# Performance work log

Measured on AMD Instinct MI355X. Metric: run time of the kernel, lower is better.

Reference implementation:

```python
import jax, jax.numpy as jnp
import numpy as np

H1, H2 = 80, 100

def _lstm_layer(x, W_ih, W_hh, b_ih, b_hh):
    # x: [B,T,D]; W_ih: [4H,D]; W_hh: [4H,H]; gate order i,f,g,o (PyTorch)
    B, T, _ = x.shape
    H = W_hh.shape[1]
    xg = jnp.einsum('btd,gd->btg', x, W_ih) + b_ih + b_hh  # [B,T,4H]
    def step(carry, xg_t):
        h, c = carry
        g = xg_t + h @ W_hh.T
        i = jax.nn.sigmoid(g[:, 0*H:1*H])
        f = jax.nn.sigmoid(g[:, 1*H:2*H])
        gg = jnp.tanh(g[:, 2*H:3*H])
        o = jax.nn.sigmoid(g[:, 3*H:4*H])
        c = f * c + i * gg
        h = o * jnp.tanh(c)
        return (h, c), h
    h0 = jnp.zeros((B, H), x.dtype)
    (_, _), hs = jax.lax.scan(step, (h0, h0), jnp.swapaxes(xg, 0, 1))
    return jnp.swapaxes(hs, 0, 1)  # [B,T,H]

def setup_inputs() -> dict:
    key = jax.random.key(0)
    ks = jax.random.split(key, 13)
    def u(k, shape, fan):
        s = 1.0 / np.sqrt(fan)
        return jax.random.uniform(k, shape, jnp.float32, -s, s)
    B, T = 1024, 512
    return {
        'x': jax.random.normal(ks[0], (B, T, 1), jnp.float32),
        'W_ih1': u(ks[1], (4*H1, 1), H1), 'W_hh1': u(ks[2], (4*H1, H1), H1),
        'b_ih1': u(ks[3], (4*H1,), H1), 'b_hh1': u(ks[4], (4*H1,), H1),
        'W_ih2': u(ks[5], (4*H2, H1), H2), 'W_hh2': u(ks[6], (4*H2, H2), H2),
        'b_ih2': u(ks[7], (4*H2,), H2), 'b_hh2': u(ks[8], (4*H2,), H2),
        'W_l1': u(ks[9], (10, 100), 100), 'b_l1': u(ks[10], (10,), 100),
        'W_l2': u(ks[11], (1, 10), 10), 'b_l2': u(ks[12], (1,), 10),
    }

def reference(x, W_ih1, W_hh1, b_ih1, b_hh1, W_ih2, W_hh2, b_ih2, b_hh2, W_l1, b_l1, W_l2, b_l2):
    h = jax.nn.relu(_lstm_layer(x, W_ih1, W_hh1, b_ih1, b_hh1))
    h = jax.nn.relu(_lstm_layer(h, W_ih2, W_hh2, b_ih2, b_hh2))
    h = h[:, -1, :]                       # [B,100]
    h = jax.nn.relu(h @ W_l1.T + b_l1)    # [B,10]
    return h @ W_l2.T + b_l2              # [B,1]
```

## Files before the change

kernel.cpp:

```cpp
#include <hip/hip_runtime.h>
#include <hip/hip_bf16.h>

#define T_STEPS 512
#define BATCH   1024
#define HD1     80
#define HD2     100
#define NB2     16

#define NKT1    3
#define NUT1    5
#define NT1     (4 * NUT1)
#define NKT2    6
#define NUT2    7
#define NT2     (4 * NUT2)
#define W1F_DW  (NT1 * NKT1 * 64 * 4)
#define W2F_DW  (NT2 * NKT2 * 64 * 4)

typedef _Float16 half2_t __attribute__((ext_vector_type(2)));
typedef _Float16 f16x4   __attribute__((ext_vector_type(4)));
typedef _Float16 f16x8   __attribute__((ext_vector_type(8)));
typedef float    f32x4   __attribute__((ext_vector_type(4)));

union HU { unsigned int u; half2_t h; };
static __device__ __forceinline__ unsigned int packh(float a, float b) {
    HU x; x.h.x = (_Float16)a; x.h.y = (_Float16)b; return x.u;
}

static __device__ __forceinline__ float sigm(float z) {
    return __builtin_amdgcn_rcpf(1.f + __expf(-z));
}
static __device__ __forceinline__ float tanhf_(float z) {
    return fmaf(2.f, __builtin_amdgcn_rcpf(1.f + __expf(-2.f * z)), -1.f);
}

__global__ __launch_bounds__(256)
void prep_kernel(const float* __restrict__ W_hh1,
                 const float* __restrict__ W_ih2,
                 const float* __restrict__ W_hh2,
                 const float* __restrict__ W_ih1,
                 const float* __restrict__ b_ih1,
                 const float* __restrict__ b_hh1,
                 const float* __restrict__ b_ih2,
                 const float* __restrict__ b_hh2,
                 unsigned int* __restrict__ w1f,
                 unsigned int* __restrict__ w2f)
{
    int i = blockIdx.x * 256 + threadIdx.x;
    if (i < W1F_DW) {
        int H  = 2 * i;
        int s  = H & 7;
        int l  = (H >> 3) & 63;
        int ri = H >> 9;
        int kt = ri % NKT1;
        int tile = ri / NKT1;
        int g  = tile / NUT1, j = tile % NUT1;
        int r  = g * HD1 + j * 16 + (l & 15);
        int k  = kt * 32 + (l >> 4) * 8 + s;
        auto val1 = [&](int kk) -> float {
            if (kk < HD1) return W_hh1[r * HD1 + kk];
            if (kk == HD1) return b_ih1[r] + b_hh1[r];
            if (kk == HD1 + 1) return W_ih1[r];
            return 0.f;
        };
        w1f[i] = packh(val1(k), val1(k + 1));
    } else if (i < W1F_DW + W2F_DW) {
        int d  = i - W1F_DW;
        int H  = 2 * d;
        int s  = H & 7;
        int l  = (H >> 3) & 63;
        int ri = H >> 9;
        int kt = ri % NKT2;
        int tile = ri / NKT2;
        int g  = tile / NUT2, j = tile % NUT2;
        int up = j * 16 + (l & 15);
        int k  = kt * 32 + (l >> 4) * 8 + s;
        float v0 = 0.f, v1 = 0.f;
        if (up < HD2) {
            int r = g * HD2 + up;
            auto val2 = [&](int kk) -> float {
                if (kk < HD1) return W_ih2[r * HD1 + kk];
                if (kk < HD1 + HD2) return W_hh2[r * HD2 + (kk - HD1)];
                if (kk == HD1 + HD2) return b_ih2[r] + b_hh2[r];
                return 0.f;
            };
            v0 = val2(k); v1 = val2(k + 1);
        }
        w2f[d] = packh(v0, v1);
    }
}

__global__ __launch_bounds__(768, 1)
void lstm_fused(const float* __restrict__ x,
                const _Float16* __restrict__ w1f,
                const _Float16* __restrict__ w2f,
                float* __restrict__ h2last)
{
    const int tid = threadIdx.x;
    const int l   = tid & 63;
    const int wv  = tid >> 6;
    const int b0  = blockIdx.x * NB2;
    const int bt  = l & 15;
    const int ro  = (l >> 4) << 2;
    const bool isL2 = (wv < 7);
    const int lane_base = ((l >> 4) << 7) + (bt << 3);

    __shared__ float    xs[T_STEPS * NB2];
    __shared__ _Float16 h1b[2][12 * 128];
    __shared__ _Float16 Hb[2][24 * 128];

    f16x8 a[4][NKT2];
    if (isL2) {
#pragma unroll
        for (int g = 0; g < 4; g++)
#pragma unroll
            for (int kt = 0; kt < NKT2; kt++)
                a[g][kt] = *(const volatile f16x8*)(w2f +
                    ((size_t)((g * NUT2 + wv) * NKT2 + kt) * 64 + l) * 8);
    } else {
        const int j1 = wv - 7;
#pragma unroll
        for (int g = 0; g < 4; g++)
#pragma unroll
            for (int kt = 0; kt < NKT1; kt++)
                a[g][kt] = *(const volatile f16x8*)(w1f +
                    ((size_t)((g * NUT1 + j1) * NKT1 + kt) * 64 + l) * 8);
    }

    const int u0 = isL2 ? (wv * 16 + ro) : ((wv - 7) * 16 + ro);
    const bool worker = isL2 ? (u0 < HD2) : true;

    float c[4] = {0.f, 0.f, 0.f, 0.f};

    for (int i = tid; i < 2 * 12 * 128 / 2; i += 768) ((unsigned int*)h1b)[i] = 0u;
    for (int i = tid; i < 2 * 24 * 128 / 2; i += 768) ((unsigned int*)Hb)[i]  = 0u;
    for (int idx = tid; idx < T_STEPS * NB2; idx += 768) {
        int tt = idx & (T_STEPS - 1), bb = idx >> 9;
        xs[tt * NB2 + bb] = x[((size_t)(b0 + bb)) * T_STEPS + tt];
    }
    __syncthreads();
    if (tid < NB2) {
        h1b[0][10 * 128 + tid * 8 + 0] = (_Float16)1.f;
        h1b[1][10 * 128 + tid * 8 + 0] = (_Float16)1.f;
        h1b[1][10 * 128 + tid * 8 + 1] =
            (_Float16)x[((size_t)(b0 + tid)) * T_STEPS];
        Hb[0][22 * 128 + tid * 8 + 4] = (_Float16)1.f;
        Hb[1][22 * 128 + tid * 8 + 4] = (_Float16)1.f;
    }
    __syncthreads();

#pragma unroll 2
    for (int i = 0; i <= T_STEPS; i++) {
        const int rp = (i - 1) & 1;
        const int wp = i & 1;
        if (isL2) {
            if (i >= 1) {
                const _Float16* bp = &Hb[rp][0] + lane_base;
                f16x8 bfr[NKT2];
#pragma unroll
                for (int kt = 0; kt < NKT2; kt++)
                    bfr[kt] = *(const f16x8*)(bp + kt * 512);
                f32x4 acc[4];
#pragma unroll
                for (int g = 0; g < 4; g++) {
                    f32x4 z4 = {0.f, 0.f, 0.f, 0.f};
#pragma unroll
                    for (int kt = 0; kt < NKT2; kt++)
                        z4 = __builtin_amdgcn_mfma_f32_16x16x32_f16(
                                 a[g][kt], bfr[kt], z4, 0, 0, 0);
                    acc[g] = z4;
                }
                if (worker) {
                    f16x4 hh;
#pragma unroll
                    for (int r = 0; r < 4; r++) {
                        float gi = sigm(acc[0][r]);
                        float gf = sigm(acc[1][r]);
                        float gg = tanhf_(acc[2][r]);
                        float go = sigm(acc[3][r]);
                        c[r] = fmaf(gf, c[r], gi * gg);
                        float h = go * tanhf_(c[r]);
                        hh[r] = (_Float16)h;
                        if (i == T_STEPS)
                            h2last[(size_t)(b0 + bt) * HD2 + u0 + r] = fmaxf(h, 0.f);
                    }
                    int k0 = HD1 + u0;
                    *(f16x4*)&Hb[wp][(k0 >> 3) * 128 + (bt << 3) + (k0 & 7)] = hh;
                }
            }
        } else {
            if (i < T_STEPS) {
                const _Float16* bp = &h1b[rp][0] + lane_base;
                f16x8 bfr[NKT1];
#pragma unroll
                for (int kt = 0; kt < NKT1; kt++)
                    bfr[kt] = *(const f16x8*)(bp + kt * 512);
                f32x4 acc[4];
#pragma unroll
                for (int g = 0; g < 4; g++) {
                    f32x4 z4 = {0.f, 0.f, 0.f, 0.f};
#pragma unroll
                    for (int kt = 0; kt < NKT1; kt++)
                        z4 = __builtin_amdgcn_mfma_f32_16x16x32_f16(
                                 a[g][kt], bfr[kt], z4, 0, 0, 0);
                    acc[g] = z4;
                }
                f16x4 hraw, hrel;
#pragma unroll
                for (int r = 0; r < 4; r++) {
                    float gi = sigm(acc[0][r]);
                    float gf = sigm(acc[1][r]);
                    float gg = tanhf_(acc[2][r]);
                    float go = sigm(acc[3][r]);
                    c[r] = fmaf(gf, c[r], gi * gg);
                    float h = go * tanhf_(c[r]);
                    hraw[r] = (_Float16)h;
                    hrel[r] = (_Float16)fmaxf(h, 0.f);
                }
                int off = (u0 >> 3) * 128 + (bt << 3) + (u0 & 7);
                *(f16x4*)&h1b[wp][off] = hraw;
                *(f16x4*)&Hb[wp][off]  = hrel;
                if (wv == 7 && l < NB2 && i + 1 < T_STEPS)
                    h1b[wp][10 * 128 + l * 8 + 1] =
                        (_Float16)xs[(i + 1) * NB2 + l];
            }
        }
        __syncthreads();
    }
}

__global__ __launch_bounds__(64)
void head_kernel(const float* __restrict__ h2last,
                 const float* __restrict__ W_l1,
                 const float* __restrict__ b_l1,
                 const float* __restrict__ W_l2,
                 const float* __restrict__ b_l2,
                 float* __restrict__ out)
{
    int b = blockIdx.x * 64 + threadIdx.x;
    if (b >= BATCH) return;
    const float* h = h2last + (size_t)b * HD2;
    float o = b_l2[0];
#pragma unroll
    for (int u = 0; u < 10; u++) {
        float s = b_l1[u];
#pragma unroll
        for (int k = 0; k < HD2; k++) s = fmaf(W_l1[u * HD2 + k], h[k], s);
        o = fmaf(W_l2[u], fmaxf(s, 0.f), o);
    }
    out[b] = o;
}

extern "C" void kernel_launch(void* const* d_in, const int* in_sizes, int n_in,
                              void* d_out, int out_size, void* d_ws, size_t ws_size,
                              hipStream_t stream)
{
    const float* x     = (const float*)d_in[0];
    const float* W_ih1 = (const float*)d_in[1];
    const float* W_hh1 = (const float*)d_in[2];
    const float* b_ih1 = (const float*)d_in[3];
    const float* b_hh1 = (const float*)d_in[4];
    const float* W_ih2 = (const float*)d_in[5];
    const float* W_hh2 = (const float*)d_in[6];
    const float* b_ih2 = (const float*)d_in[7];
    const float* b_hh2 = (const float*)d_in[8];
    const float* W_l1  = (const float*)d_in[9];
    const float* b_l1  = (const float*)d_in[10];
    const float* W_l2  = (const float*)d_in[11];
    const float* b_l2  = (const float*)d_in[12];
    float* out = (float*)d_out;

    char* p = (char*)d_ws;
    float* h2last      = (float*)p;        p += (size_t)BATCH * HD2 * 4;
    unsigned int* w1fu = (unsigned int*)p; p += (size_t)W1F_DW * 4;
    unsigned int* w2fu = (unsigned int*)p;

    int prep_n = W1F_DW + W2F_DW;
    hipLaunchKernelGGL(prep_kernel, dim3((prep_n + 255) / 256), dim3(256), 0, stream,
                       W_hh1, W_ih2, W_hh2, W_ih1, b_ih1, b_hh1, b_ih2, b_hh2,
                       w1fu, w2fu);
    hipLaunchKernelGGL(lstm_fused, dim3(BATCH / NB2), dim3(768), 0, stream,
                       x, (const _Float16*)w1fu, (const _Float16*)w2fu, h2last);
    hipLaunchKernelGGL(head_kernel, dim3(BATCH / 64), dim3(64), 0, stream,
                       h2last, W_l1, b_l1, W_l2, b_l2, out);
}
```

Measured before the change: 681.2 us.

## Split LSTM layers into producer/consumer blocks pipelined through global memory with flags

Replaces the single fused block per batch group, which ran both LSTM layers in lockstep with 12 waves, with separate layer-1 and layer-2 blocks. The layer-1 block writes ReLU'd hidden states to global memory in 16-step chunks and publishes a per-chunk ready flag. The layer-2 block has a loader wave that polls these flags and prefetches chunks into double-buffered LDS using global_load_lds. The aim is to let each layer run on its own CU with less per-step barrier contention, doubling the number of blocks to use more of the GPU. The cost is extra global traffic, spin-wait latency, and a dependence on producer and consumer blocks being co-resident to avoid deadlock.

```diff
diff --git a/kernel.cpp b/kernel.cpp
--- a/kernel.cpp
+++ b/kernel.cpp
@@ -6,6 +6,7 @@
 #define HD1     80
 #define HD2     100
 #define NB2     16
+#define NGRP    (BATCH / NB2)
 
 #define NKT1    3
 #define NUT1    5
@@ -16,6 +17,10 @@
 #define W1F_DW  (NT1 * NKT1 * 64 * 4)
 #define W2F_DW  (NT2 * NKT2 * 64 * 4)
 
+#define CH      16
+#define NCH     (T_STEPS / CH)
+#define LINE_H  1280
+
 typedef _Float16 half2_t __attribute__((ext_vector_type(2)));
 typedef _Float16 f16x4   __attribute__((ext_vector_type(4)));
 typedef _Float16 f16x8   __attribute__((ext_vector_type(8)));
@@ -31,6 +36,12 @@
 }
 static __device__ __forceinline__ float tanhf_(float z) {
     return fmaf(2.f, __builtin_amdgcn_rcpf(1.f + __expf(-2.f * z)), -1.f);
+}
+
+static __device__ __forceinline__ void gld_lds16(const void* g, void* l) {
+    __builtin_amdgcn_global_load_lds(
+        (const __attribute__((address_space(1))) unsigned int*)g,
+        (__attribute__((address_space(3))) unsigned int*)l, 16, 0, 0);
 }
 
 __global__ __launch_bounds__(256)
@@ -43,7 +54,8 @@
                  const float* __restrict__ b_ih2,
                  const float* __restrict__ b_hh2,
                  unsigned int* __restrict__ w1f,
-                 unsigned int* __restrict__ w2f)
+                 unsigned int* __restrict__ w2f,
+                 int* __restrict__ flags)
 {
     int i = blockIdx.x * 256 + threadIdx.x;
     if (i < W1F_DW) {
@@ -86,88 +98,167 @@
             v0 = val2(k); v1 = val2(k + 1);
         }
         w2f[d] = packh(v0, v1);
+    } else if (i < W1F_DW + W2F_DW + NGRP * NCH) {
+        flags[i - W1F_DW - W2F_DW] = 0;
     }
 }
 
-__global__ __launch_bounds__(768, 1)
-void lstm_fused(const float* __restrict__ x,
+__global__ __launch_bounds__(512, 1)
+void lstm_split(const float* __restrict__ x,
                 const _Float16* __restrict__ w1f,
                 const _Float16* __restrict__ w2f,
+                _Float16* __restrict__ h1g,
+                int* __restrict__ flags,
                 float* __restrict__ h2last)
 {
     const int tid = threadIdx.x;
     const int l   = tid & 63;
     const int wv  = tid >> 6;
-    const int b0  = blockIdx.x * NB2;
     const int bt  = l & 15;
     const int ro  = (l >> 4) << 2;
-    const bool isL2 = (wv < 7);
     const int lane_base = ((l >> 4) << 7) + (bt << 3);
 
     __shared__ float    xs[T_STEPS * NB2];
     __shared__ _Float16 h1b[2][12 * 128];
-    __shared__ _Float16 Hb[2][24 * 128];
-
-    f16x8 a[4][NKT2];
-    if (isL2) {
-#pragma unroll
-        for (int g = 0; g < 4; g++)
-#pragma unroll
-            for (int kt = 0; kt < NKT2; kt++)
-                a[g][kt] = *(const volatile f16x8*)(w2f +
-                    ((size_t)((g * NUT2 + wv) * NKT2 + kt) * 64 + l) * 8);
-    } else {
-        const int j1 = wv - 7;
-#pragma unroll
-        for (int g = 0; g < 4; g++)
-#pragma unroll
-            for (int kt = 0; kt < NKT1; kt++)
-                a[g][kt] = *(const volatile f16x8*)(w1f +
-                    ((size_t)((g * NUT1 + j1) * NKT1 + kt) * 64 + l) * 8);
-    }
-
-    const int u0 = isL2 ? (wv * 16 + ro) : ((wv - 7) * 16 + ro);
-    const bool worker = isL2 ? (u0 < HD2) : true;
-
-    float c[4] = {0.f, 0.f, 0.f, 0.f};
-
-    for (int i = tid; i < 2 * 12 * 128 / 2; i += 768) ((unsigned int*)h1b)[i] = 0u;
-    for (int i = tid; i < 2 * 24 * 128 / 2; i += 768) ((unsigned int*)Hb)[i]  = 0u;
-    for (int idx = tid; idx < T_STEPS * NB2; idx += 768) {
-        int tt = idx & (T_STEPS - 1), bb = idx >> 9;
-        xs[tt * NB2 + bb] = x[((size_t)(b0 + bb)) * T_STEPS + tt];
-    }
-    __syncthreads();
-    if (tid < NB2) {
-        h1b[0][10 * 128 + tid * 8 + 0] = (_Float16)1.f;
-        h1b[1][10 * 128 + tid * 8 + 0] = (_Float16)1.f;
-        h1b[1][10 * 128 + tid * 8 + 1] =
-            (_Float16)x[((size_t)(b0 + tid)) * T_STEPS];
-        Hb[0][22 * 128 + tid * 8 + 4] = (_Float16)1.f;
-        Hb[1][22 * 128 + tid * 8 + 4] = (_Float16)1.f;
-    }
-    __syncthreads();
+    __shared__ _Float16 chunkbuf[2][CH * LINE_H];
+    __shared__ _Float16 h2buf[2][14 * 128];
+
+    if (blockIdx.x < NGRP) {
+        const int g  = blockIdx.x;
+        const int b0 = g * NB2;
+        const bool workerW = (wv < 5);
+        const int u0 = wv * 16 + ro;
+
+        f16x8 a[4][NKT1];
+        if (workerW) {
+#pragma unroll
+            for (int gg = 0; gg < 4; gg++)
+#pragma unroll
+                for (int kt = 0; kt < NKT1; kt++)
+                    a[gg][kt] = *(const volatile f16x8*)(w1f +
+                        ((size_t)((gg * NUT1 + wv) * NKT1 + kt) * 64 + l) * 8);
+        }
+        float c[4] = {0.f, 0.f, 0.f, 0.f};
+
+        for (int i = tid; i < 2 * 12 * 128 / 2; i += 512) ((unsigned int*)h1b)[i] = 0u;
+        for (int idx = tid; idx < T_STEPS * NB2; idx += 512) {
+            int tt = idx & (T_STEPS - 1), bb = idx >> 9;
+            xs[tt * NB2 + bb] = x[((size_t)(b0 + bb)) * T_STEPS + tt];
+        }
+        __syncthreads();
+        if (tid < NB2) {
+            h1b[0][10 * 128 + tid * 8 + 0] = (_Float16)1.f;
+            h1b[1][10 * 128 + tid * 8 + 0] = (_Float16)1.f;
+            h1b[1][10 * 128 + tid * 8 + 1] = (_Float16)xs[0 * NB2 + tid];
+        }
+        __syncthreads();
 
 #pragma unroll 2
-    for (int i = 0; i <= T_STEPS; i++) {
-        const int rp = (i - 1) & 1;
-        const int wp = i & 1;
-        if (isL2) {
-            if (i >= 1) {
-                const _Float16* bp = &Hb[rp][0] + lane_base;
-                f16x8 bfr[NKT2];
-#pragma unroll
-                for (int kt = 0; kt < NKT2; kt++)
+        for (int i = 0; i < T_STEPS; i++) {
+            const int rp = (i - 1) & 1, wp = i & 1;
+            if (workerW) {
+                const _Float16* bp = &h1b[rp][0] + lane_base;
+                f16x8 bfr[NKT1];
+#pragma unroll
+                for (int kt = 0; kt < NKT1; kt++)
                     bfr[kt] = *(const f16x8*)(bp + kt * 512);
                 f32x4 acc[4];
 #pragma unroll
-                for (int g = 0; g < 4; g++) {
+                for (int gg = 0; gg < 4; gg++) {
+                    f32x4 z4 = {0.f, 0.f, 0.f, 0.f};
+#pragma unroll
+                    for (int kt = 0; kt < NKT1; kt++)
+                        z4 = __builtin_amdgcn_mfma_f32_16x16x32_f16(
+                                 a[gg][kt], bfr[kt], z4, 0, 0, 0);
+                    acc[gg] = z4;
+                }
+                f16x4 hraw, hrel;
+#pragma unroll
+                for (int r = 0; r < 4; r++) {
+                    float gi = sigm(acc[0][r]);
+                    float gf = sigm(acc[1][r]);
+                    float gg2 = tanhf_(acc[2][r]);
+                    float go = sigm(acc[3][r]);
+                    c[r] = fmaf(gf, c[r], gi * gg2);
+                    float h = go * tanhf_(c[r]);
+                    hraw[r] = (_Float16)h;
+                    hrel[r] = (_Float16)fmaxf(h, 0.f);
+                }
+                int off = (u0 >> 3) * 128 + (bt << 3) + (u0 & 7);
+                *(f16x4*)&h1b[wp][off] = hraw;
+                size_t goff = (((size_t)(i >> 4) * NGRP + g) * CH + (i & 15)) * LINE_H + off;
+                *(f16x4*)(h1g + goff) = hrel;
+            } else if (wv == 5 && l < NB2 && i + 1 < T_STEPS) {
+                h1b[wp][10 * 128 + l * 8 + 1] = (_Float16)xs[(i + 1) * NB2 + l];
+            }
+            __syncthreads();
+            if ((i & 15) == 15 && tid == 0) {
+                __threadfence();
+                __hip_atomic_store(&flags[g * NCH + (i >> 4)], 1,
+                                   __ATOMIC_RELEASE, __HIP_MEMORY_SCOPE_AGENT);
+            }
+        }
+    } else {
+        const int g  = blockIdx.x - NGRP;
+        const int b0 = g * NB2;
+        const bool workerWave = (wv < 7);
+        const int u0 = wv * 16 + ro;
+        const bool worker = workerWave && (u0 < HD2);
+
+        f16x8 a[4][NKT2];
+        if (workerWave) {
+#pragma unroll
+            for (int gg = 0; gg < 4; gg++)
+#pragma unroll
+                for (int kt = 0; kt < NKT2; kt++)
+                    a[gg][kt] = *(const volatile f16x8*)(w2f +
+                        ((size_t)((gg * NUT2 + wv) * NKT2 + kt) * 64 + l) * 8);
+        }
+        float c[4] = {0.f, 0.f, 0.f, 0.f};
+
+        for (int i = tid; i < 2 * 14 * 128 / 2; i += 512) ((unsigned int*)h2buf)[i] = 0u;
+        __syncthreads();
+        if (tid < NB2) {
+            h2buf[0][12 * 128 + tid * 8 + 4] = (_Float16)1.f;
+            h2buf[1][12 * 128 + tid * 8 + 4] = (_Float16)1.f;
+        }
+        if (wv == 7) {
+            while (__hip_atomic_load(&flags[g * NCH], __ATOMIC_ACQUIRE,
+                                     __HIP_MEMORY_SCOPE_AGENT) == 0)
+                __builtin_amdgcn_s_sleep(8);
+            const _Float16* gsrc = h1g + (size_t)g * (CH * LINE_H) + l * 8;
+#pragma unroll
+            for (int q = 0; q < 40; q++)
+                gld_lds16(gsrc + q * 512, &chunkbuf[0][q * 512]);
+        }
+        __syncthreads();
+
+        int cb = 0;
+        bool nissued = false;
+        for (int i = 0; i < T_STEPS; i++) {
+            const int tc = i & (CH - 1);
+            const int ch = i >> 4;
+            if (workerWave) {
+                const _Float16* ck  = &chunkbuf[cb][tc * LINE_H];
+                const _Float16* h2p = &h2buf[i & 1][0];
+                f16x8 bfr[NKT2];
+#pragma unroll
+                for (int kt = 0; kt < NKT2; kt++) {
+                    int gi = kt * 4 + (l >> 4);
+                    const _Float16* src = (gi < 10)
+                        ? (ck + gi * 128 + (bt << 3))
+                        : (h2p + (gi - 10) * 128 + (bt << 3));
+                    bfr[kt] = *(const f16x8*)src;
+                }
+                f32x4 acc[4];
+#pragma unroll
+                for (int gg = 0; gg < 4; gg++) {
                     f32x4 z4 = {0.f, 0.f, 0.f, 0.f};
 #pragma unroll
                     for (int kt = 0; kt < NKT2; kt++)
                         z4 = __builtin_amdgcn_mfma_f32_16x16x32_f16(
-                                 a[g][kt], bfr[kt], z4, 0, 0, 0);
-                    acc[g] = z4;
+                                 a[gg][kt], bfr[kt], z4, 0, 0, 0);
+                    acc[gg] = z4;
                 }
                 if (worker) {
                     f16x4 hh;
@@ -175,56 +266,42 @@
                     for (int r = 0; r < 4; r++) {
                         float gi = sigm(acc[0][r]);
                         float gf = sigm(acc[1][r]);
-                        float gg = tanhf_(acc[2][r]);
+                        float gg2 = tanhf_(acc[2][r]);
                         float go = sigm(acc[3][r]);
-                        c[r] = fmaf(gf, c[r], gi * gg);
+                        c[r] = fmaf(gf, c[r], gi * gg2);
                         float h = go * tanhf_(c[r]);
                         hh[r] = (_Float16)h;
-                        if (i == T_STEPS)
+                        if (i == T_STEPS - 1)
                             h2last[(size_t)(b0 + bt) * HD2 + u0 + r] = fmaxf(h, 0.f);
                     }
                     int k0 = HD1 + u0;
-                    *(f16x4*)&Hb[wp][(k0 >> 3) * 128 + (bt << 3) + (k0 & 7)] = hh;
+                    *(f16x4*)&h2buf[(i + 1) & 1]
+                        [((k0 >> 3) - 10) * 128 + (bt << 3) + (k0 & 7)] = hh;
+                }
+            } else {
+                if (!nissued && ch + 1 < NCH) {
+                    bool rdy = (__hip_atomic_load(&flags[g * NCH + ch + 1],
+                                    __ATOMIC_ACQUIRE, __HIP_MEMORY_SCOPE_AGENT) != 0);
+                    if (tc == CH - 1 && !rdy) {
+                        while (__hip_atomic_load(&flags[g * NCH + ch + 1],
+                                   __ATOMIC_ACQUIRE, __HIP_MEMORY_SCOPE_AGENT) == 0)
+                            __builtin_amdgcn_s_sleep(8);
+                        rdy = true;
+                    }
+                    if (rdy) {
+                        const _Float16* gsrc = h1g +
+                            ((size_t)(ch + 1) * NGRP + g) * (CH * LINE_H) + l * 8;
+                        _Float16* dst = &chunkbuf[cb ^ 1][0];
+#pragma unroll
+                        for (int q = 0; q < 40; q++)
+                            gld_lds16(gsrc + q * 512, dst + q * 512);
+                        nissued = true;
+                    }
                 }
             }
-        } else {
-            if (i < T_STEPS) {
-                const _Float16* bp = &h1b[rp][0] + lane_base;
-                f16x8 bfr[NKT1];
-#pragma unroll
-                for (int kt = 0; kt < NKT1; kt++)
-                    bfr[kt] = *(const f16x8*)(bp + kt * 512);
-                f32x4 acc[4];
-#pragma unroll
-                for (int g = 0; g < 4; g++) {
-                    f32x4 z4 = {0.f, 0.f, 0.f, 0.f};
-#pragma unroll
-                    for (int kt = 0; kt < NKT1; kt++)
-                        z4 = __builtin_amdgcn_mfma_f32_16x16x32_f16(
-                                 a[g][kt], bfr[kt], z4, 0, 0, 0);
-                    acc[g] = z4;
-                }
-                f16x4 hraw, hrel;
-#pragma unroll
-                for (int r = 0; r < 4; r++) {
-                    float gi = sigm(acc[0][r]);
-                    float gf = sigm(acc[1][r]);
-                    float gg = tanhf_(acc[2][r]);
-                    float go = sigm(acc[3][r]);
-                    c[r] = fmaf(gf, c[r], gi * gg);
-                    float h = go * tanhf_(c[r]);
-                    hraw[r] = (_Float16)h;
-                    hrel[r] = (_Float16)fmaxf(h, 0.f);
-                }
-                int off = (u0 >> 3) * 128 + (bt << 3) + (u0 & 7);
-                *(f16x4*)&h1b[wp][off] = hraw;
-                *(f16x4*)&Hb[wp][off]  = hrel;
-                if (wv == 7 && l < NB2 && i + 1 < T_STEPS)
-                    h1b[wp][10 * 128 + l * 8 + 1] =
-                        (_Float16)xs[(i + 1) * NB2 + l];
-            }
-        }
-        __syncthreads();
+            __syncthreads();
+            if (tc == CH - 1) { cb ^= 1; nissued = false; }
+        }
     }
 }
 
@@ -272,14 +349,17 @@
     char* p = (char*)d_ws;
     float* h2last      = (float*)p;        p += (size_t)BATCH * HD2 * 4;
     unsigned int* w1fu = (unsigned int*)p; p += (size_t)W1F_DW * 4;
-    unsigned int* w2fu = (unsigned int*)p;
-
-    int prep_n = W1F_DW + W2F_DW;
+    unsigned int* w2fu = (unsigned int*)p; p += (size_t)W2F_DW * 4;
+    int* flags         = (int*)p;          p += (size_t)NGRP * NCH * 4;
+    _Float16* h1g      = (_Float16*)p;
+
+    int prep_n = W1F_DW + W2F_DW + NGRP * NCH;
     hipLaunchKernelGGL(prep_kernel, dim3((prep_n + 255) / 256), dim3(256), 0, stream,
                        W_hh1, W_ih2, W_hh2, W_ih1, b_ih1, b_hh1, b_ih2, b_hh2,
-                       w1fu, w2fu);
-    hipLaunchKernelGGL(lstm_fused, dim3(BATCH / NB2), dim3(768), 0, stream,
-                       x, (const _Float16*)w1fu, (const _Float16*)w2fu, h2last);
+                       w1fu, w2fu, flags);
+    hipLaunchKernelGGL(lstm_split, dim3(2 * NGRP), dim3(512), 0, stream,
+                       x, (const _Float16*)w1fu, (const _Float16*)w2fu,
+                       h1g, flags, h2last);
     hipLaunchKernelGGL(head_kernel, dim3(BATCH / 64), dim3(64), 0, stream,
                        h2last, W_l1, b_l1, W_l2, b_l2, out);
 }
```

New measurement: 639.7 us. -6.1%, faster.
